# Kernel optimization log

Hardware: AMD Instinct MI355X
Metric: run time of the kernel (lower is better)

## Reference

```python
import jax, jax.numpy as jnp
import numpy as np
from jax import lax

NW_LIST = [4, 8, 12]   # num_windows_list for num_windows=8
HEADS = 4
EPS = 1e-5             # BatchNorm eps (eval mode, running_mean=0, running_var=1)


def conv2d(x, w, pad):
    return lax.conv_general_dilated(x, w, (1, 1), [(pad, pad), (pad, pad)],
                                    dimension_numbers=('NCHW', 'OIHW', 'NCHW'))


def bn(x, g, b):
    # eval-mode BatchNorm with running_mean=0, running_var=1
    s = g / np.sqrt(1.0 + EPS)
    return x * s[None, :, None, None] + b[None, :, None, None]


def psa(x, q_w, k_w, v_w, proj_w):
    # multi-head spatial self-attention within a window, residual output
    B, C, h, w = x.shape
    L = h * w
    hd = C // HEADS
    q = conv2d(x, q_w, 0).reshape(B, HEADS, hd, L)
    k = conv2d(x, k_w, 0).reshape(B, HEADS, hd, L)
    v = conv2d(x, v_w, 0).reshape(B, HEADS, hd, L)
    attn = jax.nn.softmax(jnp.einsum('bhdl,bhdm->bhlm', q, k) * (hd ** -0.5), axis=-1)
    o = jnp.einsum('bhlm,bhdm->bhdl', attn, v).reshape(B, C, h, w)
    return conv2d(o, proj_w, 0) + x


def dpconv_forward(x, conv1_w, bn1_g, bn1_b, conv2_w, bn2_g, bn2_b,
                   conv3_w, bn3_g, bn3_b, pos_w, bnp_g, bnp_b,
                   q_w, k_w, v_w, proj_w):
    x1 = bn(conv2d(x, conv1_w, 0), bn1_g, bn1_b)
    chunks = jnp.split(x1, 3, axis=1)
    N, Cb, H, W = chunks[0].shape
    outs = []
    for nw, xc in zip(NW_LIST, chunks):
        sh, sw = H // nw, W // nw
        kh, kw = sh + H % nw, sw + W % nw
        hh = (np.arange(nw) * sh)[:, None] + np.arange(kh)   # [nw, kh] static indices
        ww = (np.arange(nw) * sw)[:, None] + np.arange(kw)   # [nw, kw]
        # unfold: [N,Cb,nw,kh,nw,kw] -> torch layout [N, Cb*kh*kw, L]
        p = xc[:, :, hh[:, :, None, None], ww[None, None, :, :]]
        u = p.transpose(0, 1, 3, 5, 2, 4).reshape(N, Cb * kh * kw, nw * nw)
        uw = u.reshape(-1, Cb, kh, kw)   # mirrors torch .view(-1, C, kh, kw)
        att = psa(uw, q_w, k_w, v_w, proj_w) + bn(conv2d(uw, pos_w, 1), bnp_g, bnp_b)
        y = att.reshape(N, Cb, kh, kw, nw, nw).transpose(0, 1, 4, 2, 5, 3)
        folded = jnp.zeros((N, Cb, H, W), x.dtype).at[
            :, :, hh[:, :, None, None], ww[None, None, :, :]].add(y)
        cnt = jnp.zeros((H, W), x.dtype).at[
            hh[:, :, None, None], ww[None, None, :, :]].add(
            jnp.ones((nw, kh, nw, kw), x.dtype))
        outs.append(folded / cnt[None, None])
    cat = jnp.concatenate(outs, axis=1)
    h2 = bn(conv2d(cat, conv2_w, 1), bn2_g, bn2_b) + x1
    return bn(conv2d(h2, conv3_w, 1), bn3_g, bn3_b)


def setup_inputs() -> dict:
    key = jax.random.key(0)
    ks = jax.random.split(key, 10)
    C, Cb = 192, 64
    inp = {
        'x': jax.random.normal(ks[0], (2, C, 100, 100), jnp.float32),
        'conv1_w': jax.random.normal(ks[1], (C, C, 1, 1), jnp.float32) * 0.05,
        'bn1_g': jnp.ones((C,), jnp.float32), 'bn1_b': jnp.zeros((C,), jnp.float32),
        'conv2_w': jax.random.normal(ks[2], (C, C, 3, 3), jnp.float32) * 0.05,
        'bn2_g': jnp.ones((C,), jnp.float32), 'bn2_b': jnp.zeros((C,), jnp.float32),
        'conv3_w': jax.random.normal(ks[3], (C, C, 3, 3), jnp.float32) * 0.05,
        'bn3_g': jnp.ones((C,), jnp.float32), 'bn3_b': jnp.zeros((C,), jnp.float32),
        'pos_w': jax.random.normal(ks[4], (Cb, Cb, 3, 3), jnp.float32) * 0.05,
        'bnp_g': jnp.ones((Cb,), jnp.float32), 'bnp_b': jnp.zeros((Cb,), jnp.float32),
        'q_w': jax.random.normal(ks[5], (Cb, Cb, 1, 1), jnp.float32) * 0.05,
        'k_w': jax.random.normal(ks[6], (Cb, Cb, 1, 1), jnp.float32) * 0.05,
        'v_w': jax.random.normal(ks[7], (Cb, Cb, 1, 1), jnp.float32) * 0.05,
        'proj_w': jax.random.normal(ks[8], (Cb, Cb, 1, 1), jnp.float32) * 0.05,
    }
    return inp


def reference(x, conv1_w, bn1_g, bn1_b, conv2_w, bn2_g, bn2_b,
              conv3_w, bn3_g, bn3_b, pos_w, bnp_g, bnp_b,
              q_w, k_w, v_w, proj_w):
    return dpconv_forward(x, conv1_w, bn1_g, bn1_b, conv2_w, bn2_g, bn2_b,
                          conv3_w, bn3_g, bn3_b, pos_w, bnp_g, bnp_b,
                          q_w, k_w, v_w, proj_w)
```

## Files before the change

kernel.cpp:

```cpp
#include <hip/hip_runtime.h>
#include <hip/hip_bf16.h>

#define N_ 2
#define C_ 192
#define CB_ 64
#define HW_ 100
#define PIX_ (HW_*HW_)
#define PADW_ 102
#define PADPIX_ (PADW_*PADW_)
#define KTOT_ 1728
#define KPOS_ 576
#define QSCALE_ 0.3606737602222409f

typedef __attribute__((ext_vector_type(8))) short bf16x8;
typedef __attribute__((ext_vector_type(4))) short bf16x4;
typedef __attribute__((ext_vector_type(4))) float f32x4;

#if defined(__has_builtin)
#if __has_builtin(__builtin_amdgcn_mfma_f32_16x16x16bf16_1k)
#define HAVE_MFMA16 1
#endif
#if __has_builtin(__builtin_amdgcn_exp2f)
#define EXP2(x) __builtin_amdgcn_exp2f(x)
#endif
#endif
#ifndef EXP2
#define EXP2(x) exp2f(x)
#endif

static __device__ __forceinline__ float bn_scale(float g) {
    return g * rsqrtf(1.0f + 1e-5f);
}

static __device__ __forceinline__ unsigned short f2bf(float v) {
    __hip_bfloat16 h = __float2bfloat16(v);
    return *(unsigned short*)&h;
}

__global__ __launch_bounds__(256) void x_nhwc_k(
    const float* __restrict__ in, unsigned short* __restrict__ out)
{
    int idx = blockIdx.x * 256 + threadIdx.x;
    if (idx >= N_ * 4 * PIX_) return;
    int p     = idx % PIX_;
    int chunk = (idx / PIX_) & 3;
    int n     = idx / (PIX_ * 4);
    int c0 = chunk * 48;
    const float* ip = in + ((size_t)n * C_ + c0) * PIX_ + p;
    unsigned short vals[48];
    #pragma unroll
    for (int j = 0; j < 48; ++j) vals[j] = f2bf(ip[(size_t)j * PIX_]);
    unsigned short* op = out + ((size_t)n * PIX_ + p) * 192 + c0;
    #pragma unroll
    for (int v = 0; v < 6; ++v) {
        bf16x8 pack;
        #pragma unroll
        for (int j = 0; j < 8; ++j) pack[j] = (short)vals[v * 8 + j];
        *(bf16x8*)(op + v * 8) = pack;
    }
}

__global__ __launch_bounds__(256) void conv1x1_mfma_k(
    const unsigned short* __restrict__ Xc,
    const float* __restrict__ w,
    const float* __restrict__ g, const float* __restrict__ bb,
    float* __restrict__ out)
{
    __shared__ unsigned short lds[64][72];
    int tid  = threadIdx.x;
    int lane = tid & 63;
    int wv   = tid >> 6;
    int c    = lane & 15;
    int g8   = (lane >> 4) * 8;
    int p0   = blockIdx.x * 64;
    int co0  = blockIdx.y * 64;
    int n    = blockIdx.z;

    int sp = tid >> 2;
    int sk = (tid & 3) * 8;
    int pc = min(p0 + sp, PIX_ - 1);
    const unsigned short* bp = Xc + ((size_t)n * PIX_ + pc) * 192;

    const float* arow = w + (size_t)(co0 + wv * 16 + c) * C_;

    f32x4 acc[4];
    #pragma unroll
    for (int f = 0; f < 4; ++f) acc[f] = (f32x4){0.f, 0.f, 0.f, 0.f};

    bf16x8 b0 = *(const bf16x8*)(bp + sk);
    bf16x8 b1 = *(const bf16x8*)(bp + 32 + sk);

    for (int k0 = 0; k0 < C_; k0 += 64) {
        __syncthreads();
        *(bf16x8*)(&lds[sp][sk])      = b0;
        *(bf16x8*)(&lds[sp][32 + sk]) = b1;
        __syncthreads();
        if (k0 + 64 < C_) {
            b0 = *(const bf16x8*)(bp + k0 + 64 + sk);
            b1 = *(const bf16x8*)(bp + k0 + 96 + sk);
        }
        #pragma unroll
        for (int h = 0; h < 2; ++h) {
            bf16x8 a;
            const float* ap = arow + k0 + h * 32 + g8;
            #pragma unroll
            for (int j = 0; j < 8; ++j) a[j] = (short)f2bf(ap[j]);
            #pragma unroll
            for (int f = 0; f < 4; ++f) {
                bf16x8 b = *(const bf16x8*)(&lds[f * 16 + c][h * 32 + g8]);
                acc[f] = __builtin_amdgcn_mfma_f32_16x16x32_bf16(a, b, acc[f], 0, 0, 0);
            }
        }
    }

    #pragma unroll
    for (int f = 0; f < 4; ++f) {
        int p = p0 + f * 16 + c;
        if (p < PIX_) {
            #pragma unroll
            for (int r = 0; r < 4; ++r) {
                int co = co0 + wv * 16 + (lane >> 4) * 4 + r;
                out[(size_t)(n * C_ + co) * PIX_ + p] = acc[f][r] * bn_scale(g[co]) + bb[co];
            }
        }
    }
}

__global__ __launch_bounds__(256) void wcvt_all_k(
    const float* __restrict__ pw, const float* __restrict__ w2,
    const float* __restrict__ w3,
    unsigned short* __restrict__ pwb, unsigned short* __restrict__ w2b,
    unsigned short* __restrict__ w3b)
{
    int idx = blockIdx.x * 256 + threadIdx.x;
    const int S0 = CB_ * KPOS_;
    const int S1 = S0 + C_ * KTOT_;
    const int S2 = S1 + C_ * KTOT_;
    if (idx < S0) {
        int t = idx % 9, ci = (idx / 9) % CB_, co = idx / (9 * CB_);
        pwb[(size_t)co * KPOS_ + t * CB_ + ci] = f2bf(pw[idx]);
    } else if (idx < S1) {
        int k = idx - S0;
        int t = k % 9, ci = (k / 9) % C_, co = k / (9 * C_);
        w2b[(size_t)co * KTOT_ + t * C_ + ci] = f2bf(w2[k]);
    } else if (idx < S2) {
        int k = idx - S1;
        int t = k % 9, ci = (k / 9) % C_, co = k / (9 * C_);
        w3b[(size_t)co * KTOT_ + t * C_ + ci] = f2bf(w3[k]);
    }
}

template<int NW, int SH, int KH>
__device__ __forceinline__ void gather_body(
    const float* __restrict__ x1, float* __restrict__ U, int f, int cidx)
{
    int t = f;
    int j = t % NW; t /= NW;
    int i = t % NW; t /= NW;
    int c = t % KH; t /= KH;
    int r = t % KH; t /= KH;
    int cb = t % CB_;
    int n  = t / CB_;
    int hh = i * SH + r;
    int ww = j * SH + c;
    U[f] = x1[((n * C_ + cidx * CB_ + cb) * HW_ + hh) * HW_ + ww];
}

__global__ __launch_bounds__(256) void gather_c_k(
    const float* __restrict__ x1, float* __restrict__ Uall)
{
    int gid = blockIdx.x * 256 + threadIdx.x;
    if (gid < 1280000)       gather_body<4, 25, 25>(x1, Uall,            gid,            0);
    else if (gid < 3377152)  gather_body<8, 12, 16>(x1, Uall + 1280000,  gid - 1280000,  1);
    else if (gid < 6031360)  gather_body<12, 8, 12>(x1, Uall + 3377152,  gid - 3377152,  2);
}

template<int L, int LP, int NPIX>
__device__ __forceinline__ void qkv_body(
    unsigned short (*lds)[72],
    const float* __restrict__ U,
    const float* __restrict__ qw, const float* __restrict__ kw,
    const float* __restrict__ vw,
    unsigned short* __restrict__ Q, unsigned short* __restrict__ Kt,
    unsigned short* __restrict__ V, int bid)
{
    int tid  = threadIdx.x;
    int lane = tid & 63;
    int wv   = tid >> 6;
    int c    = lane & 15;
    int g8   = (lane >> 4) * 8;
    int q0   = bid * 64;

    int sp = tid >> 2;
    int sk = (tid & 3) * 8;
    int qc = min(q0 + sp, NPIX - 1);
    int b  = qc / L, p = qc % L;
    const float* ub = U + (size_t)b * 64 * L + p;

    bf16x8 b0, b1;
    #pragma unroll
    for (int j = 0; j < 8; ++j) {
        b0[j] = (short)f2bf(ub[(size_t)(sk + j) * L]);
        b1[j] = (short)f2bf(ub[(size_t)(32 + sk + j) * L]);
    }
    __syncthreads();
    *(bf16x8*)(&lds[sp][sk])      = b0;
    *(bf16x8*)(&lds[sp][32 + sk]) = b1;
    __syncthreads();

    f32x4 acc[3][4];
    #pragma unroll
    for (int s = 0; s < 3; ++s)
        #pragma unroll
        for (int f = 0; f < 4; ++f) acc[s][f] = (f32x4){0.f, 0.f, 0.f, 0.f};

    const float* wbase[3] = {qw, kw, vw};
    #pragma unroll
    for (int s = 0; s < 3; ++s) {
        const float* arow = wbase[s] + (size_t)(wv * 16 + c) * 64;
        #pragma unroll
        for (int h = 0; h < 2; ++h) {
            bf16x8 a;
            const float* ap = arow + h * 32 + g8;
            #pragma unroll
            for (int j = 0; j < 8; ++j) a[j] = (short)f2bf(ap[j]);
            #pragma unroll
            for (int f = 0; f < 4; ++f) {
                bf16x8 bfr = *(const bf16x8*)(&lds[f * 16 + c][h * 32 + g8]);
                acc[s][f] = __builtin_amdgcn_mfma_f32_16x16x32_bf16(a, bfr, acc[s][f], 0, 0, 0);
            }
        }
    }

    #pragma unroll
    for (int f = 0; f < 4; ++f) {
        int qq = q0 + f * 16 + c;
        if (qq < NPIX) {
            int bo = qq / L, po = qq % L;
            #pragma unroll
            for (int r = 0; r < 4; ++r) {
                int co = wv * 16 + (lane >> 4) * 4 + r;
                Q[(size_t)(bo * 64 + co) * L + po] = f2bf(acc[0][f][r] * QSCALE_);
                Kt[((size_t)(bo * 4 + wv) * L + po) * 16 + ((lane >> 4) * 4 + r)] = f2bf(acc[1][f][r]);
                V[(size_t)(bo * 64 + co) * LP + po] = f2bf(acc[2][f][r]);
            }
        }
    }
}

__global__ __launch_bounds__(256) void qkv_c_k(
    const float* __restrict__ Uall,
    const float* __restrict__ qw, const float* __restrict__ kw,
    const float* __restrict__ vw,
    unsigned short* __restrict__ Qa, unsigned short* __restrict__ Ka,
    unsigned short* __restrict__ Va)
{
    __shared__ unsigned short lds[64][72];
    int bid = blockIdx.x;
    if (bid < 313)
        qkv_body<625, 632, 20000>(lds, Uall, qw, kw, vw, Qa, Ka, Va, bid);
    else if (bid < 825)
        qkv_body<256, 256, 32768>(lds, Uall + 1280000, qw, kw, vw,
                                  Qa + 1280000, Ka + 1280000, Va + 1294336, bid - 313);
    else
        qkv_body<144, 144, 41472>(lds, Uall + 3377152, qw, kw, vw,
                                  Qa + 3377152, Ka + 3377152, Va + 3391488, bid - 825);
}

template<int L, int LP, int NMT>
__device__ __forceinline__ void attn_body(
    const unsigned short* __restrict__ Q, const unsigned short* __restrict__ Kt,
    const unsigned short* __restrict__ V, unsigned short* __restrict__ O,
    int lblk, int bh)
{
    int tid  = threadIdx.x;
    int lane = tid & 63;
    int wv   = tid >> 6;
    int c    = lane & 15;
    int g    = lane >> 4;
    int b = bh >> 2, h = bh & 3;
    const unsigned short* qb = Q + (size_t)(b * 64 + h * 16) * L;
    const unsigned short* kb = Kt + (size_t)bh * L * 16;
    const unsigned short* vb = V + (size_t)(b * 64 + h * 16) * LP + (size_t)c * LP;
    unsigned short* ob = O + (size_t)(b * 64 + h * 16) * L;

    int lbase = lblk * 128 + wv * 16 + c;
    int l[2] = {lbase, lbase + 64};
    bool lval[2];
    int lc[2];
    #pragma unroll
    for (int ch = 0; ch < 2; ++ch) {
        lval[ch] = (l[ch] < L);
        lc[ch] = lval[ch] ? l[ch] : (L - 1);
    }

    f32x4 acc[2];
    float mrun[2], srun[2];
    #pragma unroll
    for (int ch = 0; ch < 2; ++ch) {
        acc[ch] = (f32x4){0.f, 0.f, 0.f, 0.f};
        mrun[ch] = -1e30f; srun[ch] = 0.f;
    }

#ifdef HAVE_MFMA16
    bf16x4 qf[2];
    #pragma unroll
    for (int ch = 0; ch < 2; ++ch)
        #pragma unroll
        for (int j = 0; j < 4; ++j) qf[ch][j] = (short)qb[(g * 4 + j) * L + lc[ch]];
#else
    bf16x8 qf[2];
    #pragma unroll
    for (int ch = 0; ch < 2; ++ch) {
        qf[ch] = (bf16x8){0,0,0,0,0,0,0,0};
        if (g < 2) {
            #pragma unroll
            for (int j = 0; j < 8; ++j) qf[ch][j] = (short)qb[(g * 8 + j) * L + lc[ch]];
        }
    }
#endif

    for (int mt = 0; mt < NMT; ++mt) {
        int m0 = mt * 64;
        bool full = (m0 + 64 <= L);

        float p[2][16];
#ifdef HAVE_MFMA16
        #pragma unroll
        for (int t = 0; t < 4; ++t) {
            int mm = full ? (m0 + c + t * 16) : min(m0 + c + t * 16, L - 1);
            bf16x4 kf = *(const bf16x4*)(kb + (size_t)mm * 16 + g * 4);
            f32x4 s0 = __builtin_amdgcn_mfma_f32_16x16x16bf16_1k(
                kf, qf[0], (f32x4){0.f,0.f,0.f,0.f}, 0, 0, 0);
            f32x4 s1 = __builtin_amdgcn_mfma_f32_16x16x16bf16_1k(
                kf, qf[1], (f32x4){0.f,0.f,0.f,0.f}, 0, 0, 0);
            #pragma unroll
            for (int r = 0; r < 4; ++r) {
                p[0][t * 4 + r] = s0[r];
                p[1][t * 4 + r] = s1[r];
            }
        }
#else
        #pragma unroll
        for (int t = 0; t < 4; ++t) {
            bf16x8 kf = (bf16x8){0,0,0,0,0,0,0,0};
            if (g < 2) {
                int mm = full ? (m0 + c + t * 16) : min(m0 + c + t * 16, L - 1);
                kf = *(const bf16x8*)(kb + (size_t)mm * 16 + g * 8);
            }
            f32x4 s0 = __builtin_amdgcn_mfma_f32_16x16x32_bf16(
                kf, qf[0], (f32x4){0.f,0.f,0.f,0.f}, 0, 0, 0);
            f32x4 s1 = __builtin_amdgcn_mfma_f32_16x16x32_bf16(
                kf, qf[1], (f32x4){0.f,0.f,0.f,0.f}, 0, 0, 0);
            #pragma unroll
            for (int r = 0; r < 4; ++r) {
                p[0][t * 4 + r] = s0[r];
                p[1][t * 4 + r] = s1[r];
            }
        }
#endif

        #pragma unroll
        for (int ch = 0; ch < 2; ++ch) {
            float tmax = -1e30f;
            #pragma unroll
            for (int t = 0; t < 4; ++t) {
                #pragma unroll
                for (int r = 0; r < 4; ++r) {
                    int m = m0 + t * 16 + g * 4 + r;
                    float v = p[ch][t * 4 + r];
                    if (!full && m >= L) v = -1e30f;
                    p[ch][t * 4 + r] = v;
                    tmax = fmaxf(tmax, v);
                }
            }
            tmax = fmaxf(tmax, __shfl_xor(tmax, 16, 64));
            tmax = fmaxf(tmax, __shfl_xor(tmax, 32, 64));
            if (!__all(tmax <= mrun[ch])) {
                float mnew = fmaxf(mrun[ch], tmax);
                float corr = EXP2(mrun[ch] - mnew);
                srun[ch] *= corr;
                #pragma unroll
                for (int r = 0; r < 4; ++r) acc[ch][r] *= corr;
                mrun[ch] = mnew;
            }
            float ps0 = 0.f, ps1 = 0.f, ps2 = 0.f, ps3 = 0.f;
            #pragma unroll
            for (int t = 0; t < 4; ++t) {
                p[ch][t * 4 + 0] = EXP2(p[ch][t * 4 + 0] - mrun[ch]); ps0 += p[ch][t * 4 + 0];
                p[ch][t * 4 + 1] = EXP2(p[ch][t * 4 + 1] - mrun[ch]); ps1 += p[ch][t * 4 + 1];
                p[ch][t * 4 + 2] = EXP2(p[ch][t * 4 + 2] - mrun[ch]); ps2 += p[ch][t * 4 + 2];
                p[ch][t * 4 + 3] = EXP2(p[ch][t * 4 + 3] - mrun[ch]); ps3 += p[ch][t * 4 + 3];
            }
            srun[ch] += (ps0 + ps1) + (ps2 + ps3);
        }

#ifdef HAVE_MFMA16
        #pragma unroll
        for (int t = 0; t < 4; ++t) {
            bf16x4 vf = *(const bf16x4*)(vb + m0 + t * 16 + g * 4);
            bf16x4 pb0, pb1;
            #pragma unroll
            for (int j = 0; j < 4; ++j) {
                pb0[j] = (short)f2bf(p[0][t * 4 + j]);
                pb1[j] = (short)f2bf(p[1][t * 4 + j]);
            }
            acc[0] = __builtin_amdgcn_mfma_f32_16x16x16bf16_1k(vf, pb0, acc[0], 0, 0, 0);
            acc[1] = __builtin_amdgcn_mfma_f32_16x16x16bf16_1k(vf, pb1, acc[1], 0, 0, 0);
        }
#else
        int hi = g >> 1;
        #pragma unroll
        for (int H = 0; H < 2; ++H) {
            bf16x8 vf = *(const bf16x8*)(vb + m0 + H * 32 + g * 8);
            #pragma unroll
            for (int ch = 0; ch < 2; ++ch) {
                bf16x8 pb;
                #pragma unroll
                for (int j = 0; j < 8; ++j) {
                    int srcLane = (((2 * g + (j >> 2)) & 3) << 4) | c;
                    float v1 = __shfl(p[ch][(H * 2) * 4 + (j & 3)], srcLane, 64);
                    float v2 = __shfl(p[ch][(H * 2 + 1) * 4 + (j & 3)], srcLane, 64);
                    pb[j] = (short)f2bf(hi ? v2 : v1);
                }
                acc[ch] = __builtin_amdgcn_mfma_f32_16x16x32_bf16(vf, pb, acc[ch], 0, 0, 0);
            }
        }
#endif
    }

    #pragma unroll
    for (int ch = 0; ch < 2; ++ch) {
        float stot = srun[ch];
        stot += __shfl_xor(stot, 16, 64);
        stot += __shfl_xor(stot, 32, 64);
        float inv = 1.f / stot;
        if (lval[ch]) {
            #pragma unroll
            for (int r = 0; r < 4; ++r)
                ob[(size_t)(g * 4 + r) * L + l[ch]] = f2bf(acc[ch][r] * inv);
        }
    }
}

__global__ __launch_bounds__(256) void attn_c_k(
    const unsigned short* __restrict__ Qa, const unsigned short* __restrict__ Ka,
    const unsigned short* __restrict__ Va, unsigned short* __restrict__ Oa)
{
    int bid = blockIdx.x;
    if (bid < 640) {
        attn_body<625, 632, 10>(Qa, Ka, Va, Oa, bid % 5, bid / 5);
    } else if (bid < 1664) {
        int k = bid - 640;
        attn_body<256, 256, 4>(Qa + 1280000, Ka + 1280000, Va + 1294336,
                               Oa + 1280000, k % 2, k / 2);
    } else {
        int k = bid - 1664;
        attn_body<144, 144, 3>(Qa + 3377152, Ka + 3377152, Va + 3391488,
                               Oa + 3377152, k % 2, k / 2);
    }
}

template<int L, int NPIX>
__device__ __forceinline__ void proj_body(
    unsigned short (*lds)[72],
    const unsigned short* __restrict__ O, const float* __restrict__ U,
    const float* __restrict__ pw, float* __restrict__ A, int bid)
{
    int tid  = threadIdx.x;
    int lane = tid & 63;
    int wv   = tid >> 6;
    int c    = lane & 15;
    int g8   = (lane >> 4) * 8;
    int q0   = bid * 64;

    int sp = tid >> 2;
    int sk = (tid & 3) * 8;
    int qc = min(q0 + sp, NPIX - 1);
    int b  = qc / L, p = qc % L;
    const unsigned short* ob = O + (size_t)b * 64 * L + p;

    bf16x8 b0, b1;
    #pragma unroll
    for (int j = 0; j < 8; ++j) {
        b0[j] = (short)ob[(size_t)(sk + j) * L];
        b1[j] = (short)ob[(size_t)(32 + sk + j) * L];
    }
    __syncthreads();
    *(bf16x8*)(&lds[sp][sk])      = b0;
    *(bf16x8*)(&lds[sp][32 + sk]) = b1;
    __syncthreads();

    f32x4 acc[4];
    #pragma unroll
    for (int f = 0; f < 4; ++f) acc[f] = (f32x4){0.f, 0.f, 0.f, 0.f};

    const float* arow = pw + (size_t)(wv * 16 + c) * 64;
    #pragma unroll
    for (int h = 0; h < 2; ++h) {
        bf16x8 a;
        const float* ap = arow + h * 32 + g8;
        #pragma unroll
        for (int j = 0; j < 8; ++j) a[j] = (short)f2bf(ap[j]);
        #pragma unroll
        for (int f = 0; f < 4; ++f) {
            bf16x8 bfr = *(const bf16x8*)(&lds[f * 16 + c][h * 32 + g8]);
            acc[f] = __builtin_amdgcn_mfma_f32_16x16x32_bf16(a, bfr, acc[f], 0, 0, 0);
        }
    }

    #pragma unroll
    for (int f = 0; f < 4; ++f) {
        int qq = q0 + f * 16 + c;
        if (qq < NPIX) {
            int bo = qq / L, po = qq % L;
            #pragma unroll
            for (int r = 0; r < 4; ++r) {
                int co = wv * 16 + (lane >> 4) * 4 + r;
                size_t oi = (size_t)(bo * 64 + co) * L + po;
                A[oi] = acc[f][r] + U[oi];
            }
        }
    }
}

__global__ __launch_bounds__(256) void proj_c_k(
    const unsigned short* __restrict__ Oa, const float* __restrict__ Uall,
    const float* __restrict__ pw, float* __restrict__ Aa)
{
    __shared__ unsigned short lds[64][72];
    int bid = blockIdx.x;
    if (bid < 313)
        proj_body<625, 20000>(lds, Oa, Uall, pw, Aa, bid);
    else if (bid < 825)
        proj_body<256, 32768>(lds, Oa + 1280000, Uall + 1280000, pw, Aa + 1280000, bid - 313);
    else
        proj_body<144, 41472>(lds, Oa + 3377152, Uall + 3377152, pw, Aa + 3377152, bid - 825);
}

template<int KH, int PW, int L>
__device__ __forceinline__ void padU_body(
    const float* __restrict__ U, unsigned short* __restrict__ Up, int idx)
{
    int pp = idx % (PW * PW);
    int b  = idx / (PW * PW);
    int xx = pp % PW, yy = pp / PW;
    bool inter = (xx >= 1 && xx <= KH && yy >= 1 && yy <= KH);
    const float* up = U + (size_t)b * 64 * L + (yy - 1) * KH + (xx - 1);
    unsigned short vals[64];
    #pragma unroll
    for (int j = 0; j < 64; ++j) vals[j] = inter ? f2bf(up[(size_t)j * L]) : 0;
    unsigned short* op = Up + (size_t)idx * 64;
    #pragma unroll
    for (int v = 0; v < 8; ++v) {
        bf16x8 pack;
        #pragma unroll
        for (int j = 0; j < 8; ++j) pack[j] = (short)vals[v * 8 + j];
        *(bf16x8*)(op + v * 8) = pack;
    }
}

__global__ __launch_bounds__(256) void padU_c_k(
    const float* __restrict__ Uall, unsigned short* __restrict__ Upa)
{
    int idx = blockIdx.x * 256 + threadIdx.x;
    if (idx < 23328)        padU_body<25, 27, 625>(Uall,            Upa,            idx);
    else if (idx < 64800)   padU_body<16, 18, 256>(Uall + 1280000,  Upa + 1492992,  idx - 23328);
    else if (idx < 121248)  padU_body<12, 14, 144>(Uall + 3377152,  Upa + 4147200,  idx - 64800);
}

template<int L, int PW, int KH, int NPIX>
__device__ __forceinline__ void posconv_body(
    unsigned short (*lds)[64][72],
    const unsigned short* __restrict__ Up, const unsigned short* __restrict__ Wb,
    const float* __restrict__ g, const float* __restrict__ bb,
    float* __restrict__ A, int bid)
{
    int tid  = threadIdx.x;
    int lane = tid & 63;
    int wv   = tid >> 6;
    int c    = lane & 15;
    int g8   = (lane >> 4) * 8;
    int p0   = bid * 64;

    int sp = tid >> 2;
    int sk = (tid & 3) * 8;
    int qq0 = p0 + sp;
    int po = 0;
    if (qq0 < NPIX) {
        int b = qq0 / L, p = qq0 % L;
        po = b * PW * PW + (p / KH) * PW + (p % KH);
    }

    const unsigned short* arow = Wb + (size_t)(wv * 16 + c) * KPOS_;

    f32x4 acc[4];
    #pragma unroll
    for (int f = 0; f < 4; ++f) acc[f] = (f32x4){0.f, 0.f, 0.f, 0.f};

    const int NT = KPOS_ / 64;

    bf16x8 b0, b1, a0, a1;
    {
        const unsigned short* bp = Up + ((size_t)po << 6);
        b0 = *(const bf16x8*)(bp + sk);
        b1 = *(const bf16x8*)(bp + 32 + sk);
        *(bf16x8*)(&lds[0][sp][sk])      = b0;
        *(bf16x8*)(&lds[0][sp][32 + sk]) = b1;
    }
    {
        const unsigned short* bp = Up + ((size_t)(po + 1) << 6);
        b0 = *(const bf16x8*)(bp + sk);
        b1 = *(const bf16x8*)(bp + 32 + sk);
    }
    a0 = *(const bf16x8*)(arow + g8);
    a1 = *(const bf16x8*)(arow + 32 + g8);

    for (int t = 0; t < NT; ++t) {
        __syncthreads();
        bf16x8 bf0[4], bf1[4];
        #pragma unroll
        for (int f = 0; f < 4; ++f) {
            bf0[f] = *(const bf16x8*)(&lds[t & 1][f * 16 + c][g8]);
            bf1[f] = *(const bf16x8*)(&lds[t & 1][f * 16 + c][32 + g8]);
        }
        if (t + 1 < NT) {
            *(bf16x8*)(&lds[(t + 1) & 1][sp][sk])      = b0;
            *(bf16x8*)(&lds[(t + 1) & 1][sp][32 + sk]) = b1;
            if (t + 2 < NT) {
                int tap = t + 2;
                int toff = (tap / 3) * PW + (tap % 3);
                const unsigned short* bp = Up + ((size_t)(po + toff) << 6);
                b0 = *(const bf16x8*)(bp + sk);
                b1 = *(const bf16x8*)(bp + 32 + sk);
            }
        }
        bf16x8 a0n, a1n;
        if (t + 1 < NT) {
            a0n = *(const bf16x8*)(arow + (t + 1) * 64 + g8);
            a1n = *(const bf16x8*)(arow + (t + 1) * 64 + 32 + g8);
        }
        #pragma unroll
        for (int f = 0; f < 4; ++f) {
            acc[f] = __builtin_amdgcn_mfma_f32_16x16x32_bf16(a0, bf0[f], acc[f], 0, 0, 0);
            acc[f] = __builtin_amdgcn_mfma_f32_16x16x32_bf16(a1, bf1[f], acc[f], 0, 0, 0);
        }
        a0 = a0n; a1 = a1n;
    }

    #pragma unroll
    for (int f = 0; f < 4; ++f) {
        int q = p0 + f * 16 + c;
        if (q < NPIX) {
            int b = q / L, p = q % L;
            #pragma unroll
            for (int r = 0; r < 4; ++r) {
                int co = wv * 16 + (lane >> 4) * 4 + r;
                A[(size_t)(b * 64 + co) * L + p] += acc[f][r] * bn_scale(g[co]) + bb[co];
            }
        }
    }
}

__global__ __launch_bounds__(256) void posconv_c_k(
    const unsigned short* __restrict__ Upa, const unsigned short* __restrict__ Wb,
    const float* __restrict__ g, const float* __restrict__ bb,
    float* __restrict__ Aa)
{
    __shared__ unsigned short lds[2][64][72];
    int bid = blockIdx.x;
    if (bid < 313)
        posconv_body<625, 27, 25, 20000>(lds, Upa, Wb, g, bb, Aa, bid);
    else if (bid < 825)
        posconv_body<256, 18, 16, 32768>(lds, Upa + 1492992, Wb, g, bb, Aa + 1280000, bid - 313);
    else
        posconv_body<144, 14, 12, 41472>(lds, Upa + 4147200, Wb, g, bb, Aa + 3377152, bid - 825);
}

template<int NW, int SH, int KH>
__device__ __forceinline__ void fold_body(
    const float* __restrict__ A, float* __restrict__ cat, int idx, int cidx)
{
    int w  = idx % HW_;
    int h  = (idx / HW_) % HW_;
    int cb = (idx / PIX_) % CB_;
    int n  = idx / (PIX_ * CB_);
    int numh = h - KH + 1;
    int ilo = numh > 0 ? (numh + SH - 1) / SH : 0;
    int ihi = min(NW - 1, h / SH);
    int numw = w - KH + 1;
    int jlo = numw > 0 ? (numw + SH - 1) / SH : 0;
    int jhi = min(NW - 1, w / SH);
    float sum = 0.f;
    for (int i = ilo; i <= ihi; ++i) {
        int r = h - i * SH;
        for (int j = jlo; j <= jhi; ++j) {
            int c = w - j * SH;
            int f = ((((n * CB_ + cb) * KH + r) * KH + c) * NW + i) * NW + j;
            sum += A[f];
        }
    }
    float cnt = (float)((ihi - ilo + 1) * (jhi - jlo + 1));
    cat[((n * C_ + cidx * CB_ + cb) * HW_ + h) * HW_ + w] = sum / cnt;
}

__global__ __launch_bounds__(256) void fold_c_k(
    const float* __restrict__ Aa, float* __restrict__ cat)
{
    int idx = blockIdx.x * 256 + threadIdx.x;
    if (idx < 1280000)       fold_body<4, 25, 25>(Aa,            cat, idx,            0);
    else if (idx < 2560000)  fold_body<8, 12, 16>(Aa + 1280000,  cat, idx - 1280000,  1);
    else if (idx < 3840000)  fold_body<12, 8, 12>(Aa + 3377152,  cat, idx - 2560000,  2);
}

__global__ __launch_bounds__(256) void pad_nhwc_k(
    const float* __restrict__ in, unsigned short* __restrict__ out)
{
    int idx = blockIdx.x * 256 + threadIdx.x;
    if (idx >= N_ * 4 * PADPIX_) return;
    int pp    = idx % PADPIX_;
    int chunk = (idx / PADPIX_) & 3;
    int n     = idx / (PADPIX_ * 4);
    int xx = pp % PADW_, yy = pp / PADW_;
    int c0 = chunk * 48;
    bool inter = (xx >= 1 && xx <= HW_ && yy >= 1 && yy <= HW_);
    const float* ip = in + ((size_t)n * C_ + c0) * PIX_ + (yy - 1) * HW_ + (xx - 1);
    unsigned short vals[48];
    #pragma unroll
    for (int j = 0; j < 48; ++j) vals[j] = inter ? f2bf(ip[(size_t)j * PIX_]) : 0;
    unsigned short* op = out + ((size_t)n * PADPIX_ + pp) * 192 + c0;
    #pragma unroll
    for (int v = 0; v < 6; ++v) {
        bf16x8 pack;
        #pragma unroll
        for (int j = 0; j < 8; ++j) pack[j] = (short)vals[v * 8 + j];
        *(bf16x8*)(op + v * 8) = pack;
    }
}

__global__ __launch_bounds__(256) void ring_zero_k(unsigned short* __restrict__ Xb)
{
    int idx = blockIdx.x * 256 + threadIdx.x;
    if (idx >= N_ * 404 * 192) return;
    int cc = idx % 192;
    int rp = (idx / 192) % 404;
    int n  = idx / (192 * 404);
    int yy, xx;
    if (rp < 102)      { yy = 0;            xx = rp; }
    else if (rp < 204) { yy = 101;          xx = rp - 102; }
    else if (rp < 304) { yy = rp - 204 + 1; xx = 0; }
    else               { yy = rp - 304 + 1; xx = 101; }
    Xb[((size_t)n * PADPIX_ + yy * PADW_ + xx) * 192 + cc] = 0;
}

#define NB3_ (157*3*2)
template<bool RES, bool TOXB>
__global__ __launch_bounds__(256) void conv3x3_mfma_k(
    const unsigned short* __restrict__ Xp,
    const unsigned short* __restrict__ Wb,
    const float* __restrict__ g, const float* __restrict__ bb,
    const float* __restrict__ res, float* __restrict__ out,
    unsigned short* __restrict__ xout)
{
    __shared__ unsigned short lds[2][64][72];
    int tid  = threadIdx.x;
    int lane = tid & 63;
    int wv   = tid >> 6;
    int c    = lane & 15;
    int g8   = (lane >> 4) * 8;

    const int q = NB3_ / 8, r = NB3_ % 8;
    int gid  = blockIdx.x;
    int xcd  = gid % 8, slot = gid / 8;
    int wgid = (xcd < r) ? xcd * (q + 1) + slot
                         : r * (q + 1) + (xcd - r) * q + slot;
    int co0  = (wgid % 3) * 64;
    int rest = wgid / 3;
    int p0   = (rest % 157) * 64;
    int n    = rest / 157;

    const unsigned short* Xn = Xp + (size_t)n * PADPIX_ * 192;

    int sp = tid >> 2;
    int sk = (tid & 3) * 8;
    int pix = p0 + sp;
    int po = (pix < PIX_) ? (pix / HW_) * PADW_ + (pix % HW_) : 0;

    const unsigned short* arow = Wb + (size_t)(co0 + wv * 16 + c) * KTOT_;

    f32x4 acc[4];
    #pragma unroll
    for (int f = 0; f < 4; ++f) acc[f] = (f32x4){0.f, 0.f, 0.f, 0.f};

    const int NT = KTOT_ / 64;

    bf16x8 b0, b1, a0, a1;
    {
        const unsigned short* bp = Xn + (size_t)po * 192;
        b0 = *(const bf16x8*)(bp + sk);
        b1 = *(const bf16x8*)(bp + 32 + sk);
        *(bf16x8*)(&lds[0][sp][sk])      = b0;
        *(bf16x8*)(&lds[0][sp][32 + sk]) = b1;
    }
    {
        const unsigned short* bp = Xn + (size_t)po * 192 + 64;
        b0 = *(const bf16x8*)(bp + sk);
        b1 = *(const bf16x8*)(bp + 32 + sk);
    }
    a0 = *(const bf16x8*)(arow + g8);
    a1 = *(const bf16x8*)(arow + 32 + g8);

    for (int t = 0; t < NT; ++t) {
        __syncthreads();
        bf16x8 bf0[4], bf1[4];
        #pragma unroll
        for (int f = 0; f < 4; ++f) {
            bf0[f] = *(const bf16x8*)(&lds[t & 1][f * 16 + c][g8]);
            bf1[f] = *(const bf16x8*)(&lds[t & 1][f * 16 + c][32 + g8]);
        }
        if (t + 1 < NT) {
            *(bf16x8*)(&lds[(t + 1) & 1][sp][sk])      = b0;
            *(bf16x8*)(&lds[(t + 1) & 1][sp][32 + sk]) = b1;
            if (t + 2 < NT) {
                int k2 = (t + 2) * 64;
                int tap = k2 / 192;
                int ci0 = k2 - tap * 192;
                int toff = (tap / 3) * PADW_ + (tap % 3);
                const unsigned short* bp = Xn + (size_t)(po + toff) * 192 + ci0;
                b0 = *(const bf16x8*)(bp + sk);
                b1 = *(const bf16x8*)(bp + 32 + sk);
            }
        }
        bf16x8 a0n, a1n;
        if (t + 1 < NT) {
            a0n = *(const bf16x8*)(arow + (t + 1) * 64 + g8);
            a1n = *(const bf16x8*)(arow + (t + 1) * 64 + 32 + g8);
        }
        #pragma unroll
        for (int f = 0; f < 4; ++f) {
            acc[f] = __builtin_amdgcn_mfma_f32_16x16x32_bf16(a0, bf0[f], acc[f], 0, 0, 0);
            acc[f] = __builtin_amdgcn_mfma_f32_16x16x32_bf16(a1, bf1[f], acc[f], 0, 0, 0);
        }
        a0 = a0n; a1 = a1n;
    }

    #pragma unroll
    for (int f = 0; f < 4; ++f) {
        int p = p0 + f * 16 + c;
        if (p < PIX_) {
            if (TOXB) {
                int py = p / HW_, px = p % HW_;
                unsigned short* o = xout +
                    ((size_t)n * PADPIX_ + (py + 1) * PADW_ + (px + 1)) * 192 +
                    co0 + wv * 16 + (lane >> 4) * 4;
                ushort4 pk;
                #pragma unroll
                for (int r2 = 0; r2 < 4; ++r2) {
                    int co = co0 + wv * 16 + (lane >> 4) * 4 + r2;
                    float v = acc[f][r2] * bn_scale(g[co]) + bb[co];
                    if (RES) v += res[(size_t)(n * C_ + co) * PIX_ + p];
                    ((unsigned short*)&pk)[r2] = f2bf(v);
                }
                *(ushort4*)o = pk;
            } else {
                #pragma unroll
                for (int r2 = 0; r2 < 4; ++r2) {
                    int co = co0 + wv * 16 + (lane >> 4) * 4 + r2;
                    float v = acc[f][r2] * bn_scale(g[co]) + bb[co];
                    if (RES) v += res[(size_t)(n * C_ + co) * PIX_ + p];
                    out[(size_t)(n * C_ + co) * PIX_ + p] = v;
                }
            }
        }
    }
}

extern "C" void kernel_launch(void* const* d_in, const int* in_sizes, int n_in,
                              void* d_out, int out_size, void* d_ws, size_t ws_size,
                              hipStream_t stream) {
    const float* x       = (const float*)d_in[0];
    const float* conv1_w = (const float*)d_in[1];
    const float* bn1_g   = (const float*)d_in[2];
    const float* bn1_b   = (const float*)d_in[3];
    const float* conv2_w = (const float*)d_in[4];
    const float* bn2_g   = (const float*)d_in[5];
    const float* bn2_b   = (const float*)d_in[6];
    const float* conv3_w = (const float*)d_in[7];
    const float* bn3_g   = (const float*)d_in[8];
    const float* bn3_b   = (const float*)d_in[9];
    const float* pos_w   = (const float*)d_in[10];
    const float* bnp_g   = (const float*)d_in[11];
    const float* bnp_b   = (const float*)d_in[12];
    const float* q_w     = (const float*)d_in[13];
    const float* k_w     = (const float*)d_in[14];
    const float* v_w     = (const float*)d_in[15];
    const float* proj_w  = (const float*)d_in[16];

    float* ws = (float*)d_ws;
    float* x1   = ws;
    float* cat  = ws + 3840000;
    unsigned short* Xc    = (unsigned short*)(ws + 7680000);
    float* Uall = ws + 9600000;
    unsigned short* Oall  = (unsigned short*)(ws + 15640000);
    float* Aall = ws + 21680000;
    unsigned short* Qall  = (unsigned short*)(ws + 27720000);
    unsigned short* Ktall = (unsigned short*)(ws + 30740000);
    unsigned short* Vall  = (unsigned short*)(ws + 33760000);
    unsigned short* Upall = (unsigned short*)(ws + 36790000);
    unsigned short* pwb   = (unsigned short*)(ws + 40670000);
    unsigned short* w2b   = (unsigned short*)(ws + 40690000);
    unsigned short* w3b   = (unsigned short*)(ws + 40856000);
    unsigned short* Xb    = (unsigned short*)(ws + 41022000);
    unsigned short* Xb2   = (unsigned short*)(ws + 43020000);

    x_nhwc_k<<<(N_ * 4 * PIX_ + 255) / 256, 256, 0, stream>>>(x, Xc);
    conv1x1_mfma_k<<<dim3(157, 3, 2), 256, 0, stream>>>(Xc, conv1_w, bn1_g, bn1_b, x1);
    wcvt_all_k<<<(700416 + 255) / 256, 256, 0, stream>>>(pos_w, conv2_w, conv3_w, pwb, w2b, w3b);

    gather_c_k<<<(6031360 + 255) / 256, 256, 0, stream>>>(x1, Uall);
    qkv_c_k<<<1473, 256, 0, stream>>>(Uall, q_w, k_w, v_w, Qall, Ktall, Vall);
    attn_c_k<<<2688 + 1280, 256, 0, stream>>>(Qall, Ktall, Vall, Oall);
    proj_c_k<<<1473, 256, 0, stream>>>(Oall, Uall, proj_w, Aall);
    padU_c_k<<<(121248 + 255) / 256, 256, 0, stream>>>(Uall, Upall);
    posconv_c_k<<<1473, 256, 0, stream>>>(Upall, pwb, bnp_g, bnp_b, Aall);
    fold_c_k<<<(3840000 + 255) / 256, 256, 0, stream>>>(Aall, cat);

    pad_nhwc_k<<<(N_ * 4 * PADPIX_ + 255) / 256, 256, 0, stream>>>(cat, Xb);
    ring_zero_k<<<(N_ * 404 * 192 + 255) / 256, 256, 0, stream>>>(Xb2);
    conv3x3_mfma_k<true, true><<<NB3_, 256, 0, stream>>>(
        Xb, w2b, bn2_g, bn2_b, x1, nullptr, Xb2);
    conv3x3_mfma_k<false, false><<<NB3_, 256, 0, stream>>>(
        Xb2, w3b, bn3_g, bn3_b, nullptr, (float*)d_out, nullptr);
}
```

Measured before the change: 293.7 us.

## Fuse fold output into padded NHWC bf16 buffer and split attention tail tile

The fold kernel now writes its averaged result straight into the padded NHWC bf16 conv input, with only the border ring zeroed by a separate launch. This removes the fp32 NCHW intermediate and the full pad/transpose kernel along with its extra memory pass. Separately, the attention loop is split into full tiles without masking and one masked tail tile, which drops per-element bound checks from the main loop. The cost is that fold's bf16 stores are strided by channel (192 elements apart), so they are less coalesced than the old pad kernel's packed vector stores.

```diff
diff --git a/kernel.cpp b/kernel.cpp
--- a/kernel.cpp
+++ b/kernel.cpp
@@ -267,12 +267,135 @@
                                   Qa + 3377152, Ka + 3377152, Va + 3391488, bid - 825);
 }
 
-template<int L, int LP, int NMT>
+template<int L, int LP, bool MASK>
+__device__ __forceinline__ void attn_tile(
+    int m0, const unsigned short* __restrict__ kb,
+    const unsigned short* __restrict__ vb, int c, int g,
+#ifdef HAVE_MFMA16
+    const bf16x4* qf,
+#else
+    const bf16x8* qf,
+#endif
+    f32x4* acc, float* mrun, float* srun)
+{
+    float p[2][16];
+#ifdef HAVE_MFMA16
+    #pragma unroll
+    for (int t = 0; t < 4; ++t) {
+        int mm = m0 + c + t * 16;
+        if (MASK) mm = min(mm, L - 1);
+        bf16x4 kf = *(const bf16x4*)(kb + (size_t)mm * 16 + g * 4);
+        f32x4 s0 = __builtin_amdgcn_mfma_f32_16x16x16bf16_1k(
+            kf, qf[0], (f32x4){0.f,0.f,0.f,0.f}, 0, 0, 0);
+        f32x4 s1 = __builtin_amdgcn_mfma_f32_16x16x16bf16_1k(
+            kf, qf[1], (f32x4){0.f,0.f,0.f,0.f}, 0, 0, 0);
+        #pragma unroll
+        for (int r = 0; r < 4; ++r) {
+            p[0][t * 4 + r] = s0[r];
+            p[1][t * 4 + r] = s1[r];
+        }
+    }
+#else
+    #pragma unroll
+    for (int t = 0; t < 4; ++t) {
+        bf16x8 kf = (bf16x8){0,0,0,0,0,0,0,0};
+        if (g < 2) {
+            int mm = m0 + c + t * 16;
+            if (MASK) mm = min(mm, L - 1);
+            kf = *(const bf16x8*)(kb + (size_t)mm * 16 + g * 8);
+        }
+        f32x4 s0 = __builtin_amdgcn_mfma_f32_16x16x32_bf16(
+            kf, qf[0], (f32x4){0.f,0.f,0.f,0.f}, 0, 0, 0);
+        f32x4 s1 = __builtin_amdgcn_mfma_f32_16x16x32_bf16(
+            kf, qf[1], (f32x4){0.f,0.f,0.f,0.f}, 0, 0, 0);
+        #pragma unroll
+        for (int r = 0; r < 4; ++r) {
+            p[0][t * 4 + r] = s0[r];
+            p[1][t * 4 + r] = s1[r];
+        }
+    }
+#endif
+
+    #pragma unroll
+    for (int ch = 0; ch < 2; ++ch) {
+        float tmax = -1e30f;
+        #pragma unroll
+        for (int t = 0; t < 4; ++t) {
+            #pragma unroll
+            for (int r = 0; r < 4; ++r) {
+                float v = p[ch][t * 4 + r];
+                if (MASK) {
+                    int m = m0 + t * 16 + g * 4 + r;
+                    if (m >= L) v = -1e30f;
+                    p[ch][t * 4 + r] = v;
+                }
+                tmax = fmaxf(tmax, v);
+            }
+        }
+        tmax = fmaxf(tmax, __shfl_xor(tmax, 16, 64));
+        tmax = fmaxf(tmax, __shfl_xor(tmax, 32, 64));
+        if (!__all(tmax <= mrun[ch])) {
+            float mnew = fmaxf(mrun[ch], tmax);
+            float corr = EXP2(mrun[ch] - mnew);
+            srun[ch] *= corr;
+            #pragma unroll
+            for (int r = 0; r < 4; ++r) acc[ch][r] *= corr;
+            mrun[ch] = mnew;
+        }
+        float ps0 = 0.f, ps1 = 0.f, ps2 = 0.f, ps3 = 0.f;
+        #pragma unroll
+        for (int t = 0; t < 4; ++t) {
+            p[ch][t * 4 + 0] = EXP2(p[ch][t * 4 + 0] - mrun[ch]); ps0 += p[ch][t * 4 + 0];
+            p[ch][t * 4 + 1] = EXP2(p[ch][t * 4 + 1] - mrun[ch]); ps1 += p[ch][t * 4 + 1];
+            p[ch][t * 4 + 2] = EXP2(p[ch][t * 4 + 2] - mrun[ch]); ps2 += p[ch][t * 4 + 2];
+            p[ch][t * 4 + 3] = EXP2(p[ch][t * 4 + 3] - mrun[ch]); ps3 += p[ch][t * 4 + 3];
+        }
+        srun[ch] += (ps0 + ps1) + (ps2 + ps3);
+    }
+
+#ifdef HAVE_MFMA16
+    #pragma unroll
+    for (int t = 0; t < 4; ++t) {
+        bf16x4 vf = *(const bf16x4*)(vb + m0 + t * 16 + g * 4);
+        bf16x4 pb0, pb1;
+        #pragma unroll
+        for (int j = 0; j < 4; ++j) {
+            pb0[j] = (short)f2bf(p[0][t * 4 + j]);
+            pb1[j] = (short)f2bf(p[1][t * 4 + j]);
+        }
+        acc[0] = __builtin_amdgcn_mfma_f32_16x16x16bf16_1k(vf, pb0, acc[0], 0, 0, 0);
+        acc[1] = __builtin_amdgcn_mfma_f32_16x16x16bf16_1k(vf, pb1, acc[1], 0, 0, 0);
+    }
+#else
+    int hi = g >> 1;
+    #pragma unroll
+    for (int H = 0; H < 2; ++H) {
+        bf16x8 vf = *(const bf16x8*)(vb + m0 + H * 32 + g * 8);
+        #pragma unroll
+        for (int ch = 0; ch < 2; ++ch) {
+            bf16x8 pb;
+            #pragma unroll
+            for (int j = 0; j < 8; ++j) {
+                int srcLane = (((2 * g + (j >> 2)) & 3) << 4) | c;
+                float v1 = __shfl(p[ch][(H * 2) * 4 + (j & 3)], srcLane, 64);
+                float v2 = __shfl(p[ch][(H * 2 + 1) * 4 + (j & 3)], srcLane, 64);
+                pb[j] = (short)f2bf(hi ? v2 : v1);
+            }
+            acc[ch] = __builtin_amdgcn_mfma_f32_16x16x32_bf16(vf, pb, acc[ch], 0, 0, 0);
+        }
+    }
+#endif
+}
+
+template<int L, int LP>
 __device__ __forceinline__ void attn_body(
     const unsigned short* __restrict__ Q, const unsigned short* __restrict__ Kt,
     const unsigned short* __restrict__ V, unsigned short* __restrict__ O,
     int lblk, int bh)
 {
+    constexpr int NFULL = L / 64;
+    constexpr int TAIL  = L % 64;
+
     int tid  = threadIdx.x;
     int lane = tid & 63;
     int wv   = tid >> 6;
@@ -320,114 +443,10 @@
     }
 #endif
 
-    for (int mt = 0; mt < NMT; ++mt) {
-        int m0 = mt * 64;
-        bool full = (m0 + 64 <= L);
-
-        float p[2][16];
-#ifdef HAVE_MFMA16
-        #pragma unroll
-        for (int t = 0; t < 4; ++t) {
-            int mm = full ? (m0 + c + t * 16) : min(m0 + c + t * 16, L - 1);
-            bf16x4 kf = *(const bf16x4*)(kb + (size_t)mm * 16 + g * 4);
-            f32x4 s0 = __builtin_amdgcn_mfma_f32_16x16x16bf16_1k(
-                kf, qf[0], (f32x4){0.f,0.f,0.f,0.f}, 0, 0, 0);
-            f32x4 s1 = __builtin_amdgcn_mfma_f32_16x16x16bf16_1k(
-                kf, qf[1], (f32x4){0.f,0.f,0.f,0.f}, 0, 0, 0);
-            #pragma unroll
-            for (int r = 0; r < 4; ++r) {
-                p[0][t * 4 + r] = s0[r];
-                p[1][t * 4 + r] = s1[r];
-            }
-        }
-#else
-        #pragma unroll
-        for (int t = 0; t < 4; ++t) {
-            bf16x8 kf = (bf16x8){0,0,0,0,0,0,0,0};
-            if (g < 2) {
-                int mm = full ? (m0 + c + t * 16) : min(m0 + c + t * 16, L - 1);
-                kf = *(const bf16x8*)(kb + (size_t)mm * 16 + g * 8);
-            }
-            f32x4 s0 = __builtin_amdgcn_mfma_f32_16x16x32_bf16(
-                kf, qf[0], (f32x4){0.f,0.f,0.f,0.f}, 0, 0, 0);
-            f32x4 s1 = __builtin_amdgcn_mfma_f32_16x16x32_bf16(
-                kf, qf[1], (f32x4){0.f,0.f,0.f,0.f}, 0, 0, 0);
-            #pragma unroll
-            for (int r = 0; r < 4; ++r) {
-                p[0][t * 4 + r] = s0[r];
-                p[1][t * 4 + r] = s1[r];
-            }
-        }
-#endif
-
-        #pragma unroll
-        for (int ch = 0; ch < 2; ++ch) {
-            float tmax = -1e30f;
-            #pragma unroll
-            for (int t = 0; t < 4; ++t) {
-                #pragma unroll
-                for (int r = 0; r < 4; ++r) {
-                    int m = m0 + t * 16 + g * 4 + r;
-                    float v = p[ch][t * 4 + r];
-                    if (!full && m >= L) v = -1e30f;
-                    p[ch][t * 4 + r] = v;
-                    tmax = fmaxf(tmax, v);
-                }
-            }
-            tmax = fmaxf(tmax, __shfl_xor(tmax, 16, 64));
-            tmax = fmaxf(tmax, __shfl_xor(tmax, 32, 64));
-            if (!__all(tmax <= mrun[ch])) {
-                float mnew = fmaxf(mrun[ch], tmax);
-                float corr = EXP2(mrun[ch] - mnew);
-                srun[ch] *= corr;
-                #pragma unroll
-                for (int r = 0; r < 4; ++r) acc[ch][r] *= corr;
-                mrun[ch] = mnew;
-            }
-            float ps0 = 0.f, ps1 = 0.f, ps2 = 0.f, ps3 = 0.f;
-            #pragma unroll
-            for (int t = 0; t < 4; ++t) {
-                p[ch][t * 4 + 0] = EXP2(p[ch][t * 4 + 0] - mrun[ch]); ps0 += p[ch][t * 4 + 0];
-                p[ch][t * 4 + 1] = EXP2(p[ch][t * 4 + 1] - mrun[ch]); ps1 += p[ch][t * 4 + 1];
-                p[ch][t * 4 + 2] = EXP2(p[ch][t * 4 + 2] - mrun[ch]); ps2 += p[ch][t * 4 + 2];
-                p[ch][t * 4 + 3] = EXP2(p[ch][t * 4 + 3] - mrun[ch]); ps3 += p[ch][t * 4 + 3];
-            }
-            srun[ch] += (ps0 + ps1) + (ps2 + ps3);
-        }
-
-#ifdef HAVE_MFMA16
-        #pragma unroll
-        for (int t = 0; t < 4; ++t) {
-            bf16x4 vf = *(const bf16x4*)(vb + m0 + t * 16 + g * 4);
-            bf16x4 pb0, pb1;
-            #pragma unroll
-            for (int j = 0; j < 4; ++j) {
-                pb0[j] = (short)f2bf(p[0][t * 4 + j]);
-                pb1[j] = (short)f2bf(p[1][t * 4 + j]);
-            }
-            acc[0] = __builtin_amdgcn_mfma_f32_16x16x16bf16_1k(vf, pb0, acc[0], 0, 0, 0);
-            acc[1] = __builtin_amdgcn_mfma_f32_16x16x16bf16_1k(vf, pb1, acc[1], 0, 0, 0);
-        }
-#else
-        int hi = g >> 1;
-        #pragma unroll
-        for (int H = 0; H < 2; ++H) {
-            bf16x8 vf = *(const bf16x8*)(vb + m0 + H * 32 + g * 8);
-            #pragma unroll
-            for (int ch = 0; ch < 2; ++ch) {
-                bf16x8 pb;
-                #pragma unroll
-                for (int j = 0; j < 8; ++j) {
-                    int srcLane = (((2 * g + (j >> 2)) & 3) << 4) | c;
-                    float v1 = __shfl(p[ch][(H * 2) * 4 + (j & 3)], srcLane, 64);
-                    float v2 = __shfl(p[ch][(H * 2 + 1) * 4 + (j & 3)], srcLane, 64);
-                    pb[j] = (short)f2bf(hi ? v2 : v1);
-                }
-                acc[ch] = __builtin_amdgcn_mfma_f32_16x16x32_bf16(vf, pb, acc[ch], 0, 0, 0);
-            }
-        }
-#endif
-    }
+    for (int mt = 0; mt < NFULL; ++mt)
+        attn_tile<L, LP, false>(mt * 64, kb, vb, c, g, qf, acc, mrun, srun);
+    if (TAIL > 0)
+        attn_tile<L, LP, true>(NFULL * 64, kb, vb, c, g, qf, acc, mrun, srun);
 
     #pragma unroll
     for (int ch = 0; ch < 2; ++ch) {
@@ -449,15 +468,15 @@
 {
     int bid = blockIdx.x;
     if (bid < 640) {
-        attn_body<625, 632, 10>(Qa, Ka, Va, Oa, bid % 5, bid / 5);
+        attn_body<625, 632>(Qa, Ka, Va, Oa, bid % 5, bid / 5);
     } else if (bid < 1664) {
         int k = bid - 640;
-        attn_body<256, 256, 4>(Qa + 1280000, Ka + 1280000, Va + 1294336,
-                               Oa + 1280000, k % 2, k / 2);
+        attn_body<256, 256>(Qa + 1280000, Ka + 1280000, Va + 1294336,
+                            Oa + 1280000, k % 2, k / 2);
     } else {
         int k = bid - 1664;
-        attn_body<144, 144, 3>(Qa + 3377152, Ka + 3377152, Va + 3391488,
-                               Oa + 3377152, k % 2, k / 2);
+        attn_body<144, 144>(Qa + 3377152, Ka + 3377152, Va + 3391488,
+                            Oa + 3377152, k % 2, k / 2);
     }
 }
 
@@ -679,7 +698,7 @@
 
 template<int NW, int SH, int KH>
 __device__ __forceinline__ void fold_body(
-    const float* __restrict__ A, float* __restrict__ cat, int idx, int cidx)
+    const float* __restrict__ A, unsigned short* __restrict__ Xb, int idx, int cidx)
 {
     int w  = idx % HW_;
     int h  = (idx / HW_) % HW_;
@@ -701,41 +720,17 @@
         }
     }
     float cnt = (float)((ihi - ilo + 1) * (jhi - jlo + 1));
-    cat[((n * C_ + cidx * CB_ + cb) * HW_ + h) * HW_ + w] = sum / cnt;
+    Xb[((size_t)n * PADPIX_ + (h + 1) * PADW_ + (w + 1)) * 192 + cidx * CB_ + cb]
+        = f2bf(sum / cnt);
 }
 
 __global__ __launch_bounds__(256) void fold_c_k(
-    const float* __restrict__ Aa, float* __restrict__ cat)
+    const float* __restrict__ Aa, unsigned short* __restrict__ Xb)
 {
     int idx = blockIdx.x * 256 + threadIdx.x;
-    if (idx < 1280000)       fold_body<4, 25, 25>(Aa,            cat, idx,            0);
-    else if (idx < 2560000)  fold_body<8, 12, 16>(Aa + 1280000,  cat, idx - 1280000,  1);
-    else if (idx < 3840000)  fold_body<12, 8, 12>(Aa + 3377152,  cat, idx - 2560000,  2);
-}
-
-__global__ __launch_bounds__(256) void pad_nhwc_k(
-    const float* __restrict__ in, unsigned short* __restrict__ out)
-{
-    int idx = blockIdx.x * 256 + threadIdx.x;
-    if (idx >= N_ * 4 * PADPIX_) return;
-    int pp    = idx % PADPIX_;
-    int chunk = (idx / PADPIX_) & 3;
-    int n     = idx / (PADPIX_ * 4);
-    int xx = pp % PADW_, yy = pp / PADW_;
-    int c0 = chunk * 48;
-    bool inter = (xx >= 1 && xx <= HW_ && yy >= 1 && yy <= HW_);
-    const float* ip = in + ((size_t)n * C_ + c0) * PIX_ + (yy - 1) * HW_ + (xx - 1);
-    unsigned short vals[48];
-    #pragma unroll
-    for (int j = 0; j < 48; ++j) vals[j] = inter ? f2bf(ip[(size_t)j * PIX_]) : 0;
-    unsigned short* op = out + ((size_t)n * PADPIX_ + pp) * 192 + c0;
-    #pragma unroll
-    for (int v = 0; v < 6; ++v) {
-        bf16x8 pack;
-        #pragma unroll
-        for (int j = 0; j < 8; ++j) pack[j] = (short)vals[v * 8 + j];
-        *(bf16x8*)(op + v * 8) = pack;
-    }
+    if (idx < 1280000)       fold_body<4, 25, 25>(Aa,            Xb, idx,            0);
+    else if (idx < 2560000)  fold_body<8, 12, 16>(Aa + 1280000,  Xb, idx - 1280000,  1);
+    else if (idx < 3840000)  fold_body<12, 8, 12>(Aa + 3377152,  Xb, idx - 2560000,  2);
 }
 
 __global__ __launch_bounds__(256) void ring_zero_k(unsigned short* __restrict__ Xb)
@@ -912,6 +907,7 @@
     unsigned short* w3b   = (unsigned short*)(ws + 40856000);
     unsigned short* Xb    = (unsigned short*)(ws + 41022000);
     unsigned short* Xb2   = (unsigned short*)(ws + 43020000);
+    (void)cat;
 
     x_nhwc_k<<<(N_ * 4 * PIX_ + 255) / 256, 256, 0, stream>>>(x, Xc);
     conv1x1_mfma_k<<<dim3(157, 3, 2), 256, 0, stream>>>(Xc, conv1_w, bn1_g, bn1_b, x1);
@@ -923,9 +919,10 @@
     proj_c_k<<<1473, 256, 0, stream>>>(Oall, Uall, proj_w, Aall);
     padU_c_k<<<(121248 + 255) / 256, 256, 0, stream>>>(Uall, Upall);
     posconv_c_k<<<1473, 256, 0, stream>>>(Upall, pwb, bnp_g, bnp_b, Aall);
-    fold_c_k<<<(3840000 + 255) / 256, 256, 0, stream>>>(Aall, cat);
-
-    pad_nhwc_k<<<(N_ * 4 * PADPIX_ + 255) / 256, 256, 0, stream>>>(cat, Xb);
+
+    ring_zero_k<<<(N_ * 404 * 192 + 255) / 256, 256, 0, stream>>>(Xb);
+    fold_c_k<<<(3840000 + 255) / 256, 256, 0, stream>>>(Aall, Xb);
+
     ring_zero_k<<<(N_ * 404 * 192 + 255) / 256, 256, 0, stream>>>(Xb2);
     conv3x3_mfma_k<true, true><<<NB3_, 256, 0, stream>>>(
         Xb, w2b, bn2_g, bn2_b, x1, nullptr, Xb2);
```

After: 295.1 us. Within noise of the previous version (+0.5%).
